# Performance work log

Hardware: AMD Instinct MI355X
Metric: run time of the kernel (lower is better)

The kernel has to match this reference:

```python
import jax, jax.numpy as jnp
import numpy as np

B, D_MODEL, HID, N_BINS, DEPTH = 524288, 128, 16, 256, 8


def setup_inputs() -> dict:
    key = jax.random.key(0)
    ks = jax.random.split(key, 8)
    s_in = 1.0 / np.sqrt(D_MODEL)
    s_h = 1.0 / np.sqrt(HID)
    return {
        "hidden_state": jax.random.normal(ks[0], (B, D_MODEL), dtype=jnp.float32),
        # params stored as [in, out] so y = x @ W + b (equivalent to torch Linear)
        "W_in": jax.random.uniform(ks[1], (D_MODEL, HID), jnp.float32, -s_in, s_in),
        "b_in": jax.random.uniform(ks[2], (HID,), jnp.float32, -s_in, s_in),
        "embed": jax.random.normal(ks[3], (N_BINS, HID), dtype=jnp.float32),
        "W_mlp": jax.random.uniform(ks[4], (HID, HID), jnp.float32, -s_h, s_h),
        "b_mlp": jax.random.uniform(ks[5], (HID,), jnp.float32, -s_h, s_h),
        "W_out": jax.random.uniform(ks[6], (HID, N_BINS), jnp.float32, -s_h, s_h),
        "b_out": jax.random.uniform(ks[7], (N_BINS,), jnp.float32, -s_h, s_h),
    }


def reference(hidden_state, W_in, b_in, embed, W_mlp, b_mlp, W_out, b_out):
    # eval-mode forward (deterministic argmax path of AddrNet)
    h = hidden_state @ W_in + b_in  # [B, HID]
    bins = []
    for _ in range(DEPTH):  # depth=8: fixed tiny structural loop
        logits = h @ W_out + b_out          # [B, N_BINS]
        idx = jnp.argmax(logits, axis=-1)   # [B] int
        h = h + embed[idx]                  # conditioning on chosen bin
        h = jax.nn.silu(h @ W_mlp + b_mlp)
        bins.append(idx)
    return jnp.stack(bins, axis=1)  # [B, DEPTH] int32/int64 indices
```

## Files before the change

### kernel.cpp

```cpp
#include <hip/hip_runtime.h>
#include <math.h>


constexpr int BATCH  = 524288;
constexpr int DM     = 128;
constexpr int H      = 16;
constexpr int NB     = 256;
constexpr int DEPTHN = 8;

constexpr int BLOCK = 512;
constexpr int NWAVE = BLOCK / 64;
constexpr int STG   = 17;

typedef float v2f    __attribute__((ext_vector_type(2)));
typedef float f32x4  __attribute__((ext_vector_type(4)));
typedef int   i32x4  __attribute__((ext_vector_type(4)));
typedef short bf16x8 __attribute__((ext_vector_type(8)));

__device__ __forceinline__ unsigned bf16_rne(float f) {
    unsigned u = __builtin_bit_cast(unsigned, f);
    return (u + 0x7fffu + ((u >> 16) & 1u)) >> 16;
}
__device__ __forceinline__ float bf16_to_f(unsigned b) {
    return __builtin_bit_cast(float, b << 16);
}

__device__ __forceinline__ float np_expf(float x) {
    const float LOG2E = 1.442695040888963407f;
    const float C1    = 0.693359375f;
    const float C2    = -2.12194440e-4f;
    float q = rintf(x * LOG2E);
    float r = __builtin_fmaf(q, -C1, x);
    r = __builtin_fmaf(q, -C2, r);
    float p = 1.9875691500E-4f;
    p = __builtin_fmaf(p, r, 1.3981999507E-3f);
    p = __builtin_fmaf(p, r, 8.3334519073E-3f);
    p = __builtin_fmaf(p, r, 4.1665795894E-2f);
    p = __builtin_fmaf(p, r, 1.6666665459E-1f);
    p = __builtin_fmaf(p, r, 5.0000001201E-1f);
    p = __builtin_fmaf(p, r * r, r);
    p = p + 1.0f;
    if (x > 88.72283935546875f)      return INFINITY;
    if (x < -103.97208404541015625f) return 0.0f;
    return ldexpf(p, (int)q);
}

__global__ void addrnet_prep_kernel(const float* __restrict__ W_out,
                                    const float* __restrict__ W_mlp,
                                    float* __restrict__ ws) {
    int t = threadIdx.x;
    for (int i = t; i < NB * H; i += 256) {
        int p = i >> 5, r = i & 31;
        int k = r >> 1, hh = r & 1;
        ws[i] = W_out[k * NB + (2 * p + hh)];
    }
    {
        int ii = t >> 4, k = t & 15;
        ws[NB * H + ii * H + k] = W_mlp[k * H + ii];
    }
}

__global__ __launch_bounds__(BLOCK, 4) void addrnet_r21_kernel(
    const float* __restrict__ x,
    const float* __restrict__ W_in,
    const float* __restrict__ b_in,
    const float* __restrict__ embed,
    const float* __restrict__ b_mlp,
    const float* __restrict__ b_out,
    const float* __restrict__ W_out,
    const float* __restrict__ ws,
    int* __restrict__ out)
{
#pragma clang fp contract(off)
    __shared__ __align__(16) int   sA[16][64][4];
    __shared__ __align__(16) int   sStage[NWAVE][64 * STG];
    __shared__ __align__(16) float sBias[NB];

    const int tid = threadIdx.x;
    const int ln  = tid & 63;
    const int wid = tid >> 6;

    for (int slot = tid; slot < 16 * 64; slot += BLOCK) {
        int bt = slot >> 6, l = slot & 63;
        int m  = 16 * bt + (l & 15);
        int k0 = (l >> 4) * 8;
        for (int j = 0; j < 4; ++j) {
            unsigned e2[2];
            for (int e = 0; e < 2; ++e) {
                int k  = k0 + 2 * j + e;
                int kk = k & 15;
                float w = W_out[kk * NB + m];
                unsigned whi = bf16_rne(w);
                unsigned wlo = bf16_rne(w - bf16_to_f(whi));
                e2[e] = (k < 16) ? whi : wlo;
            }
            sA[bt][l][j] = (int)(e2[0] | (e2[1] << 16));
        }
    }
    if (tid < NB) sBias[tid] = b_out[tid];
    __syncthreads();

    const float* WM = ws + NB * H;
    const v2f*   WP = reinterpret_cast<const v2f*>(ws);

    const int row = blockIdx.x * BLOCK + tid;

    float h[H];
#pragma unroll
    for (int j = 0; j < H; ++j) h[j] = 0.0f;
    const float4* xr = reinterpret_cast<const float4*>(x + (size_t)row * DM);
    for (int k4 = 0; k4 < DM / 4; ++k4) {
        float4 v = xr[k4];
        const float* w0 = &W_in[(k4 * 4 + 0) * H];
        const float* w1 = &W_in[(k4 * 4 + 1) * H];
        const float* w2 = &W_in[(k4 * 4 + 2) * H];
        const float* w3 = &W_in[(k4 * 4 + 3) * H];
#pragma unroll
        for (int j = 0; j < H; ++j) {
            float a = h[j];
            a = a + v.x * w0[j];
            a = a + v.y * w1[j];
            a = a + v.z * w2[j];
            a = a + v.w * w3[j];
            h[j] = a;
        }
    }
#pragma unroll
    for (int j = 0; j < H; ++j) h[j] = h[j] + b_in[j];

    int* o = out + (size_t)row * DEPTHN;
    int* stme = &sStage[wid][ln * STG];
    const int binbase = (ln >> 4) * 4;

    for (int d = 0; d < DEPTHN; ++d) {
        float m01 = fmaxf(fabsf(h[0]), fabsf(h[1]));
        float m23 = fmaxf(fabsf(h[2]), fabsf(h[3]));
        float m45 = fmaxf(fabsf(h[4]), fabsf(h[5]));
        float m67 = fmaxf(fabsf(h[6]), fabsf(h[7]));
        float m89 = fmaxf(fabsf(h[8]), fabsf(h[9]));
        float mab = fmaxf(fabsf(h[10]), fabsf(h[11]));
        float mcd = fmaxf(fabsf(h[12]), fabsf(h[13]));
        float mef = fmaxf(fabsf(h[14]), fabsf(h[15]));
        float hmax = fmaxf(fmaxf(fmaxf(m01, m23), fmaxf(m45, m67)),
                           fmaxf(fmaxf(m89, mab), fmaxf(mcd, mef)));
        const float EPS2 = 6e-4f * hmax + 1e-5f;

        int dw[16];
#pragma unroll
        for (int i = 0; i < 8; ++i) {
            unsigned a  = bf16_rne(h[2 * i]);
            unsigned b  = bf16_rne(h[2 * i + 1]);
            unsigned la = bf16_rne(h[2 * i]     - bf16_to_f(a));
            unsigned lb = bf16_rne(h[2 * i + 1] - bf16_to_f(b));
            dw[i]     = (int)(a  | (b  << 16));
            dw[8 + i] = (int)(la | (lb << 16));
        }
#pragma unroll
        for (int i = 0; i < 16; ++i) stme[i] = dw[i];

        bf16x8 bfr[4];
#pragma unroll
        for (int g = 0; g < 4; ++g) {
            const int* p = &sStage[wid][((ln & 15) + 16 * g) * STG + (ln >> 4) * 4];
            i32x4 v = {p[0], p[1], p[2], p[3]};
            bfr[g] = __builtin_bit_cast(bf16x8, v);
        }

        float mx0 = -INFINITY, sec0 = -INFINITY, t30 = -INFINITY; int gb0 = 0, i20 = 0;
        float mx1 = -INFINITY, sec1 = -INFINITY, t31 = -INFINITY; int gb1 = 0, i21 = 0;
        float mx2 = -INFINITY, sec2 = -INFINITY, t32 = -INFINITY; int gb2 = 0, i22 = 0;
        float mx3 = -INFINITY, sec3 = -INFINITY, t33 = -INFINITY; int gb3 = 0, i23 = 0;

#define INS(MX, GB, SEC, I2, T3, V, BIN)                                   \
        {                                                                  \
            float v_ = (V); int b_ = (BIN);                                \
            T3 = fmaxf(T3, fminf(SEC, v_));                                \
            bool c1 = v_ > MX;                                             \
            bool c2 = v_ > SEC;                                            \
            I2 = c1 ? GB : (c2 ? b_ : I2);                                 \
            GB = c1 ? b_ : GB;                                             \
            SEC = __builtin_amdgcn_fmed3f(MX, SEC, v_);                    \
            MX = fmaxf(MX, v_);                                            \
        }

        for (int bt = 0; bt < 16; ++bt) {
            i32x4 a0i = *reinterpret_cast<const i32x4*>(&sA[bt][ln][0]);
            i32x4 a1i = *reinterpret_cast<const i32x4*>(&sA[bt][ln ^ 32][0]);
            bf16x8 a0 = __builtin_bit_cast(bf16x8, a0i);
            bf16x8 a1 = __builtin_bit_cast(bf16x8, a1i);
            f32x4 bias4 = *reinterpret_cast<const f32x4*>(&sBias[16 * bt + binbase]);
            int bin0 = 16 * bt + binbase;
#pragma unroll
            for (int g = 0; g < 4; ++g) {
                f32x4 acc = bias4;
                acc = __builtin_amdgcn_mfma_f32_16x16x32_bf16(a0, bfr[g], acc, 0, 0, 0);
                acc = __builtin_amdgcn_mfma_f32_16x16x32_bf16(a1, bfr[g], acc, 0, 0, 0);
                if (g == 0) {
                    INS(mx0, gb0, sec0, i20, t30, acc[0], bin0 + 0);
                    INS(mx0, gb0, sec0, i20, t30, acc[1], bin0 + 1);
                    INS(mx0, gb0, sec0, i20, t30, acc[2], bin0 + 2);
                    INS(mx0, gb0, sec0, i20, t30, acc[3], bin0 + 3);
                } else if (g == 1) {
                    INS(mx1, gb1, sec1, i21, t31, acc[0], bin0 + 0);
                    INS(mx1, gb1, sec1, i21, t31, acc[1], bin0 + 1);
                    INS(mx1, gb1, sec1, i21, t31, acc[2], bin0 + 2);
                    INS(mx1, gb1, sec1, i21, t31, acc[3], bin0 + 3);
                } else if (g == 2) {
                    INS(mx2, gb2, sec2, i22, t32, acc[0], bin0 + 0);
                    INS(mx2, gb2, sec2, i22, t32, acc[1], bin0 + 1);
                    INS(mx2, gb2, sec2, i22, t32, acc[2], bin0 + 2);
                    INS(mx2, gb2, sec2, i22, t32, acc[3], bin0 + 3);
                } else {
                    INS(mx3, gb3, sec3, i23, t33, acc[0], bin0 + 0);
                    INS(mx3, gb3, sec3, i23, t33, acc[1], bin0 + 1);
                    INS(mx3, gb3, sec3, i23, t33, acc[2], bin0 + 2);
                    INS(mx3, gb3, sec3, i23, t33, acc[3], bin0 + 3);
                }
            }
        }
#undef INS

        float kmx = -INFINITY, ksec = -INFINITY, kt3 = -INFINITY;
        int kgb = 0, ki2 = 0;
#define MERGE_KEEP(MX, GB, SEC, I2, T3, G)                                 \
        {                                                                  \
            float mx_ = MX, sec_ = SEC, t3_ = T3; int gb_ = GB, i2_ = I2;  \
            _Pragma("unroll")                                              \
            for (int s = 16; s <= 32; s <<= 1) {                           \
                float pmx = __shfl_xor(mx_, s);                            \
                int   pgb = __shfl_xor(gb_, s);                            \
                float pse = __shfl_xor(sec_, s);                           \
                int   pi2 = __shfl_xor(i2_, s);                            \
                float pt3 = __shfl_xor(t3_, s);                            \
                bool t  = pmx > mx_;                                       \
                float nmx = t ? pmx : mx_;  int ngb = t ? pgb : gb_;       \
                float lmx = t ? mx_ : pmx;  int lgb = t ? gb_ : pgb;       \
                float wse = t ? pse : sec_; int wsi = t ? pi2 : i2_;       \
                bool u  = lmx > wse;                                       \
                float nse = u ? lmx : wse;  int ni2 = u ? lgb : wsi;       \
                float c3  = u ? wse : lmx;                                 \
                float lse = t ? sec_ : pse;                                \
                float nt3 = fmaxf(fmaxf(c3, lse), fmaxf(t3_, pt3));        \
                mx_ = nmx; gb_ = ngb; sec_ = nse; i2_ = ni2; t3_ = nt3;    \
            }                                                              \
            bool own = ((ln >> 4) == (G));                                 \
            kmx = own ? mx_ : kmx;   kgb = own ? gb_ : kgb;                \
            ksec = own ? sec_ : ksec; ki2 = own ? i2_ : ki2;               \
            kt3 = own ? t3_ : kt3;                                         \
        }
        MERGE_KEEP(mx0, gb0, sec0, i20, t30, 0)
        MERGE_KEEP(mx1, gb1, sec1, i21, t31, 1)
        MERGE_KEEP(mx2, gb2, sec2, i22, t32, 2)
        MERGE_KEEP(mx3, gb3, sec3, i23, t33, 3)
#undef MERGE_KEEP

        int bi;
        if (kmx - kt3 <= EPS2) {
            float bb2 = -INFINITY;
            int bj = 0;
            for (int p = 0; p < NB / 2; ++p) {
                const v2f* wr = &WP[p * H];
                float a0 = 0.0f, a1 = 0.0f;
#pragma unroll
                for (int k = 0; k < H; ++k) {
                    v2f w = wr[k];
                    a0 = a0 + h[k] * w.x;
                    a1 = a1 + h[k] * w.y;
                }
                a0 = a0 + b_out[2 * p];
                a1 = a1 + b_out[2 * p + 1];
                if (a0 > bb2) { bb2 = a0; bj = 2 * p; }
                if (a1 > bb2) { bb2 = a1; bj = 2 * p + 1; }
            }
            bi = bj;
        } else if (kmx - ksec <= EPS2) {
            int lo  = kgb < ki2 ? kgb : ki2;
            int hi2 = kgb < ki2 ? ki2 : kgb;
            float El = 0.0f, Eh = 0.0f;
            {
                const float* wr = ws + (lo >> 1) * 32 + (lo & 1);
#pragma unroll
                for (int k = 0; k < H; ++k) El = El + h[k] * wr[2 * k];
                El = El + b_out[lo];
            }
            {
                const float* wr = ws + (hi2 >> 1) * 32 + (hi2 & 1);
#pragma unroll
                for (int k = 0; k < H; ++k) Eh = Eh + h[k] * wr[2 * k];
                Eh = Eh + b_out[hi2];
            }
            bi = (Eh > El) ? hi2 : lo;
        } else {
            bi = kgb;
        }
        o[d] = bi;

        {
            const float4* e = reinterpret_cast<const float4*>(embed + bi * H);
#pragma unroll
            for (int q4 = 0; q4 < 4; ++q4) {
                float4 ev = e[q4];
                h[q4 * 4 + 0] = h[q4 * 4 + 0] + ev.x;
                h[q4 * 4 + 1] = h[q4 * 4 + 1] + ev.y;
                h[q4 * 4 + 2] = h[q4 * 4 + 2] + ev.z;
                h[q4 * 4 + 3] = h[q4 * 4 + 3] + ev.w;
            }
        }

        float hn[H];
#pragma unroll
        for (int i = 0; i < H; ++i) {
            const float* wr = &WM[i * H];
            float acc = 0.0f;
#pragma unroll
            for (int k = 0; k < H; ++k) acc = acc + h[k] * wr[k];
            acc = acc + b_mlp[i];
            float e = np_expf(-acc);
            float s = 1.0f / (1.0f + e);
            hn[i] = acc * s;
        }
#pragma unroll
        for (int i = 0; i < H; ++i) h[i] = hn[i];
    }
}

extern "C" void kernel_launch(void* const* d_in, const int* in_sizes, int n_in,
                              void* d_out, int out_size, void* d_ws, size_t ws_size,
                              hipStream_t stream) {
    const float* x     = (const float*)d_in[0];
    const float* W_in  = (const float*)d_in[1];
    const float* b_in  = (const float*)d_in[2];
    const float* embed = (const float*)d_in[3];
    const float* W_mlp = (const float*)d_in[4];
    const float* b_mlp = (const float*)d_in[5];
    const float* W_out = (const float*)d_in[6];
    const float* b_out = (const float*)d_in[7];
    int* out  = (int*)d_out;
    float* ws = (float*)d_ws;

    addrnet_prep_kernel<<<1, 256, 0, stream>>>(W_out, W_mlp, ws);

    dim3 grid(BATCH / BLOCK);
    dim3 block(BLOCK);
    addrnet_r21_kernel<<<grid, block, 0, stream>>>(x, W_in, b_in, embed,
                                                   b_mlp, b_out, W_out, ws, out);
}
```

Baseline: 616.2 us.

## Replace top-3 tracking argmax with two-pass max-then-threshold candidate scan

Replaces the per-element top-3 insertion network and the heavy 5-value shuffle merge with two passes over the MFMA logits. The first pass computes only the per-row max. The second recomputes the logits and records the min and max bin index within an error threshold of that max, so a unique candidate is accepted directly and any tie falls back to the exact fp32 scan. It also buffers the 8 output indices and writes them as two int4 stores, and lowers the occupancy hint from 4 to 3 blocks per CU. The trade is doubled MFMA work per depth step and more fp32 fallbacks (the two-candidate refinement path is removed) against far fewer VALU select operations.

```diff
diff --git a/kernel.cpp b/kernel.cpp
--- a/kernel.cpp
+++ b/kernel.cpp
@@ -60,7 +60,7 @@
     }
 }
 
-__global__ __launch_bounds__(BLOCK, 4) void addrnet_r21_kernel(
+__global__ __launch_bounds__(BLOCK, 3) void addrnet_r22_kernel(
     const float* __restrict__ x,
     const float* __restrict__ W_in,
     const float* __restrict__ b_in,
@@ -128,9 +128,9 @@
 #pragma unroll
     for (int j = 0; j < H; ++j) h[j] = h[j] + b_in[j];
 
-    int* o = out + (size_t)row * DEPTHN;
     int* stme = &sStage[wid][ln * STG];
     const int binbase = (ln >> 4) * 4;
+    int bins_[DEPTHN];
 
     for (int d = 0; d < DEPTHN; ++d) {
         float m01 = fmaxf(fabsf(h[0]), fabsf(h[1]));
@@ -143,7 +143,6 @@
         float mef = fmaxf(fabsf(h[14]), fabsf(h[15]));
         float hmax = fmaxf(fmaxf(fmaxf(m01, m23), fmaxf(m45, m67)),
                            fmaxf(fmaxf(m89, mab), fmaxf(mcd, mef)));
-        const float EPS2 = 6e-4f * hmax + 1e-5f;
 
         int dw[16];
 #pragma unroll
@@ -166,23 +165,41 @@
             bfr[g] = __builtin_bit_cast(bf16x8, v);
         }
 
-        float mx0 = -INFINITY, sec0 = -INFINITY, t30 = -INFINITY; int gb0 = 0, i20 = 0;
-        float mx1 = -INFINITY, sec1 = -INFINITY, t31 = -INFINITY; int gb1 = 0, i21 = 0;
-        float mx2 = -INFINITY, sec2 = -INFINITY, t32 = -INFINITY; int gb2 = 0, i22 = 0;
-        float mx3 = -INFINITY, sec3 = -INFINITY, t33 = -INFINITY; int gb3 = 0, i23 = 0;
-
-#define INS(MX, GB, SEC, I2, T3, V, BIN)                                   \
-        {                                                                  \
-            float v_ = (V); int b_ = (BIN);                                \
-            T3 = fmaxf(T3, fminf(SEC, v_));                                \
-            bool c1 = v_ > MX;                                             \
-            bool c2 = v_ > SEC;                                            \
-            I2 = c1 ? GB : (c2 ? b_ : I2);                                 \
-            GB = c1 ? b_ : GB;                                             \
-            SEC = __builtin_amdgcn_fmed3f(MX, SEC, v_);                    \
-            MX = fmaxf(MX, v_);                                            \
-        }
-
+        float mxg[4] = {-INFINITY, -INFINITY, -INFINITY, -INFINITY};
+        for (int bt = 0; bt < 16; ++bt) {
+            i32x4 a0i = *reinterpret_cast<const i32x4*>(&sA[bt][ln][0]);
+            i32x4 a1i = *reinterpret_cast<const i32x4*>(&sA[bt][ln ^ 32][0]);
+            bf16x8 a0 = __builtin_bit_cast(bf16x8, a0i);
+            bf16x8 a1 = __builtin_bit_cast(bf16x8, a1i);
+            f32x4 bias4 = *reinterpret_cast<const f32x4*>(&sBias[16 * bt + binbase]);
+#pragma unroll
+            for (int g = 0; g < 4; ++g) {
+                f32x4 acc = bias4;
+                acc = __builtin_amdgcn_mfma_f32_16x16x32_bf16(a0, bfr[g], acc, 0, 0, 0);
+                acc = __builtin_amdgcn_mfma_f32_16x16x32_bf16(a1, bfr[g], acc, 0, 0, 0);
+                float q01 = fmaxf(acc[0], acc[1]);
+                float q23 = fmaxf(acc[2], acc[3]);
+                mxg[g] = fmaxf(mxg[g], fmaxf(q01, q23));
+            }
+        }
+#pragma unroll
+        for (int g = 0; g < 4; ++g) {
+            float m = mxg[g];
+            m = fmaxf(m, __shfl_xor(m, 16));
+            m = fmaxf(m, __shfl_xor(m, 32));
+            mxg[g] = m;
+        }
+        float thr[4];
+#pragma unroll
+        for (int g = 0; g < 4; ++g) {
+            float hsrc = __shfl(hmax, (ln & 15) + 16 * g);
+            thr[g] = mxg[g] - (6e-4f * hsrc + 1e-5f);
+        }
+
+        asm volatile("" ::: "memory");
+
+        int imn[4] = {1023, 1023, 1023, 1023};
+        int imx[4] = {-1, -1, -1, -1};
         for (int bt = 0; bt < 16; ++bt) {
             i32x4 a0i = *reinterpret_cast<const i32x4*>(&sA[bt][ln][0]);
             i32x4 a1i = *reinterpret_cast<const i32x4*>(&sA[bt][ln ^ 32][0]);
@@ -195,67 +212,43 @@
                 f32x4 acc = bias4;
                 acc = __builtin_amdgcn_mfma_f32_16x16x32_bf16(a0, bfr[g], acc, 0, 0, 0);
                 acc = __builtin_amdgcn_mfma_f32_16x16x32_bf16(a1, bfr[g], acc, 0, 0, 0);
-                if (g == 0) {
-                    INS(mx0, gb0, sec0, i20, t30, acc[0], bin0 + 0);
-                    INS(mx0, gb0, sec0, i20, t30, acc[1], bin0 + 1);
-                    INS(mx0, gb0, sec0, i20, t30, acc[2], bin0 + 2);
-                    INS(mx0, gb0, sec0, i20, t30, acc[3], bin0 + 3);
-                } else if (g == 1) {
-                    INS(mx1, gb1, sec1, i21, t31, acc[0], bin0 + 0);
-                    INS(mx1, gb1, sec1, i21, t31, acc[1], bin0 + 1);
-                    INS(mx1, gb1, sec1, i21, t31, acc[2], bin0 + 2);
-                    INS(mx1, gb1, sec1, i21, t31, acc[3], bin0 + 3);
-                } else if (g == 2) {
-                    INS(mx2, gb2, sec2, i22, t32, acc[0], bin0 + 0);
-                    INS(mx2, gb2, sec2, i22, t32, acc[1], bin0 + 1);
-                    INS(mx2, gb2, sec2, i22, t32, acc[2], bin0 + 2);
-                    INS(mx2, gb2, sec2, i22, t32, acc[3], bin0 + 3);
-                } else {
-                    INS(mx3, gb3, sec3, i23, t33, acc[0], bin0 + 0);
-                    INS(mx3, gb3, sec3, i23, t33, acc[1], bin0 + 1);
-                    INS(mx3, gb3, sec3, i23, t33, acc[2], bin0 + 2);
-                    INS(mx3, gb3, sec3, i23, t33, acc[3], bin0 + 3);
+#pragma unroll
+                for (int r = 0; r < 4; ++r) {
+                    bool hit = acc[r] >= thr[g];
+                    int b = bin0 + r;
+                    int clo = hit ? b : 1023;
+                    int chi = hit ? b : -1;
+                    imn[g] = clo < imn[g] ? clo : imn[g];
+                    imx[g] = chi > imx[g] ? chi : imx[g];
                 }
             }
         }
-#undef INS
-
-        float kmx = -INFINITY, ksec = -INFINITY, kt3 = -INFINITY;
-        int kgb = 0, ki2 = 0;
-#define MERGE_KEEP(MX, GB, SEC, I2, T3, G)                                 \
-        {                                                                  \
-            float mx_ = MX, sec_ = SEC, t3_ = T3; int gb_ = GB, i2_ = I2;  \
-            _Pragma("unroll")                                              \
-            for (int s = 16; s <= 32; s <<= 1) {                           \
-                float pmx = __shfl_xor(mx_, s);                            \
-                int   pgb = __shfl_xor(gb_, s);                            \
-                float pse = __shfl_xor(sec_, s);                           \
-                int   pi2 = __shfl_xor(i2_, s);                            \
-                float pt3 = __shfl_xor(t3_, s);                            \
-                bool t  = pmx > mx_;                                       \
-                float nmx = t ? pmx : mx_;  int ngb = t ? pgb : gb_;       \
-                float lmx = t ? mx_ : pmx;  int lgb = t ? gb_ : pgb;       \
-                float wse = t ? pse : sec_; int wsi = t ? pi2 : i2_;       \
-                bool u  = lmx > wse;                                       \
-                float nse = u ? lmx : wse;  int ni2 = u ? lgb : wsi;       \
-                float c3  = u ? wse : lmx;                                 \
-                float lse = t ? sec_ : pse;                                \
-                float nt3 = fmaxf(fmaxf(c3, lse), fmaxf(t3_, pt3));        \
-                mx_ = nmx; gb_ = ngb; sec_ = nse; i2_ = ni2; t3_ = nt3;    \
-            }                                                              \
-            bool own = ((ln >> 4) == (G));                                 \
-            kmx = own ? mx_ : kmx;   kgb = own ? gb_ : kgb;                \
-            ksec = own ? sec_ : ksec; ki2 = own ? i2_ : ki2;               \
-            kt3 = own ? t3_ : kt3;                                         \
-        }
-        MERGE_KEEP(mx0, gb0, sec0, i20, t30, 0)
-        MERGE_KEEP(mx1, gb1, sec1, i21, t31, 1)
-        MERGE_KEEP(mx2, gb2, sec2, i22, t32, 2)
-        MERGE_KEEP(mx3, gb3, sec3, i23, t33, 3)
-#undef MERGE_KEEP
+#pragma unroll
+        for (int g = 0; g < 4; ++g) {
+            int a = imn[g];
+            {
+                int p = __shfl_xor(a, 16); a = p < a ? p : a;
+                p = __shfl_xor(a, 32);     a = p < a ? p : a;
+            }
+            imn[g] = a;
+            int b = imx[g];
+            {
+                int p = __shfl_xor(b, 16); b = p > b ? p : b;
+                p = __shfl_xor(b, 32);     b = p > b ? p : b;
+            }
+            imx[g] = b;
+        }
+
+        const int g_own = ln >> 4;
+        int kmin = g_own == 0 ? imn[0] : g_own == 1 ? imn[1]
+                 : g_own == 2 ? imn[2] : imn[3];
+        int kmax = g_own == 0 ? imx[0] : g_own == 1 ? imx[1]
+                 : g_own == 2 ? imx[2] : imx[3];
 
         int bi;
-        if (kmx - kt3 <= EPS2) {
+        if (kmin == kmax) {
+            bi = kmin;
+        } else {
             float bb2 = -INFINITY;
             int bj = 0;
             for (int p = 0; p < NB / 2; ++p) {
@@ -273,27 +266,8 @@
                 if (a1 > bb2) { bb2 = a1; bj = 2 * p + 1; }
             }
             bi = bj;
-        } else if (kmx - ksec <= EPS2) {
-            int lo  = kgb < ki2 ? kgb : ki2;
-            int hi2 = kgb < ki2 ? ki2 : kgb;
-            float El = 0.0f, Eh = 0.0f;
-            {
-                const float* wr = ws + (lo >> 1) * 32 + (lo & 1);
-#pragma unroll
-                for (int k = 0; k < H; ++k) El = El + h[k] * wr[2 * k];
-                El = El + b_out[lo];
-            }
-            {
-                const float* wr = ws + (hi2 >> 1) * 32 + (hi2 & 1);
-#pragma unroll
-                for (int k = 0; k < H; ++k) Eh = Eh + h[k] * wr[2 * k];
-                Eh = Eh + b_out[hi2];
-            }
-            bi = (Eh > El) ? hi2 : lo;
-        } else {
-            bi = kgb;
-        }
-        o[d] = bi;
+        }
+        bins_[d] = bi;
 
         {
             const float4* e = reinterpret_cast<const float4*>(embed + bi * H);
@@ -322,6 +296,10 @@
 #pragma unroll
         for (int i = 0; i < H; ++i) h[i] = hn[i];
     }
+
+    int* o = out + (size_t)row * DEPTHN;
+    *reinterpret_cast<int4*>(o)     = make_int4(bins_[0], bins_[1], bins_[2], bins_[3]);
+    *reinterpret_cast<int4*>(o + 4) = make_int4(bins_[4], bins_[5], bins_[6], bins_[7]);
 }
 
 extern "C" void kernel_launch(void* const* d_in, const int* in_sizes, int n_in,
@@ -342,6 +320,6 @@
 
     dim3 grid(BATCH / BLOCK);
     dim3 block(BLOCK);
-    addrnet_r21_kernel<<<grid, block, 0, stream>>>(x, W_in, b_in, embed,
+    addrnet_r22_kernel<<<grid, block, 0, stream>>>(x, W_in, b_in, embed,
                                                    b_mlp, b_out, W_out, ws, out);
 }
```

New measurement: 881.8 us. 1.43x slower.
